# Kernel tuning notes

Hardware: AMD Instinct MI355X
Metric: run time of the kernel (lower is better)

Reference implementation:

```python
import jax, jax.numpy as jnp
import numpy as np

N = 16384
L = 4096  # n_locations

def setup_inputs() -> dict:
    key = jax.random.key(0)
    k1, k2, k3, k4 = jax.random.split(key, 4)
    w = jax.random.randint(k1, (N,), 0, L)
    z = jax.random.normal(k2, (N, L), dtype=jnp.float32)
    W = jax.random.normal(k3, (L, L), dtype=jnp.float32) * (1.0 / np.sqrt(L))
    b = jax.random.normal(k4, (L,), dtype=jnp.float32) * 0.01
    return {"w": w, "z": z, "W": W, "b": b}

def reference(w, z, W, b):
    # zw[i] = z[i, w[i]]
    zw = jnp.take_along_axis(z, w[:, None], axis=1)[:, 0]  # [N]
    # Original: inp = scatter(zw at column w); out = inp @ W.T + b
    # Mathematically: out[i, j] = zw[i] * W[j, w[i]] + b[j]
    out = zw[:, None] * W.T[w] + b  # [N, L]
    return out
```

## Files before the change

### kernel.cpp

```cpp
#include <hip/hip_runtime.h>

#define N_ROWS 16384
#define L_DIM  4096
#define CG     16
#define JT     1024
#define NBKT   (L_DIM / CG)
#define PITCH  (JT + 4)
#define CAP    1792

typedef float f32x4 __attribute__((ext_vector_type(4)));

__global__ __launch_bounds__(256, 2) void pnet_fused(
    const int* __restrict__ w,
    const float* __restrict__ z,
    const float* __restrict__ W,
    const float* __restrict__ b,
    float* __restrict__ out)
{
    __shared__ float tile[CG * PITCH];
    __shared__ int   list[CAP];
    __shared__ float zlist[CAP];
    __shared__ int   cnt;

    const int tid  = threadIdx.x;
    const int l0   = blockIdx.x * CG;
    const int j0   = blockIdx.y * JT;
    const int wid  = tid >> 6;
    const int lane = tid & 63;

    if (tid == 0) cnt = 0;

    f32x4 bb[4];
    #pragma unroll
    for (int k = 0; k < 4; ++k)
        bb[k] = *(const f32x4*)&b[j0 + (k * 64 + lane) * 4];

    __syncthreads();

    {
        const int q     = tid & 3;
        const int rbase = tid >> 2;
        #pragma unroll
        for (int it = 0; it < JT / 64; ++it) {
            const int r = rbase + it * 64;
            const f32x4 v = *(const f32x4*)&W[(size_t)(j0 + r) * L_DIM + l0 + 4 * q];
            tile[(4 * q + 0) * PITCH + r] = v.x;
            tile[(4 * q + 1) * PITCH + r] = v.y;
            tile[(4 * q + 2) * PITCH + r] = v.z;
            tile[(4 * q + 3) * PITCH + r] = v.w;
        }
    }

    #pragma unroll
    for (int s = 0; s < N_ROWS / 1024; ++s) {
        const int i0  = s * 1024 + tid * 4;
        const int4 wv = *(const int4*)&w[i0];
        const int vals[4] = {wv.x, wv.y, wv.z, wv.w};
        #pragma unroll
        for (int e = 0; e < 4; ++e) {
            const unsigned c = (unsigned)(vals[e] - l0);
            if (c < CG) {
                const int pos = atomicAdd(&cnt, 1);
                if (pos < CAP) list[pos] = (i0 + e) | ((int)c << 16);
            }
        }
    }

    __syncthreads();
    const int n     = cnt;
    const int nmain = n < CAP ? n : CAP;

    for (int e = tid; e < nmain; e += 256) {
        const int ent = list[e];
        const int i   = ent & 0xFFFF;
        const int c   = ent >> 16;
        zlist[e] = z[(size_t)i * L_DIM + l0 + c];
    }
    __syncthreads();

    for (int e = wid; e < nmain; e += 4) {
        const int   ent = list[e];
        const int   i   = ent & 0xFFFF;
        const int   c   = ent >> 16;
        const float zw  = zlist[e];
        const float* __restrict__ trow = &tile[c * PITCH];
        float*       __restrict__ orow = &out[(size_t)i * L_DIM + j0];
        #pragma unroll
        for (int k = 0; k < 4; ++k) {
            const int jj = (k * 64 + lane) * 4;
            const f32x4 wv4 = *(const f32x4*)&trow[jj];
            f32x4 o;
            o.x = fmaf(zw, wv4.x, bb[k].x);
            o.y = fmaf(zw, wv4.y, bb[k].y);
            o.z = fmaf(zw, wv4.z, bb[k].z);
            o.w = fmaf(zw, wv4.w, bb[k].w);
            __builtin_nontemporal_store(o, (f32x4*)&orow[jj]);
        }
    }

    if (n > CAP) {
        for (int p = 0; p < N_ROWS / 1024; ++p) {
            __syncthreads();
            if (tid == 0) cnt = 0;
            __syncthreads();
            const int i0  = p * 1024 + tid * 4;
            const int4 wv = *(const int4*)&w[i0];
            const int vals[4] = {wv.x, wv.y, wv.z, wv.w};
            #pragma unroll
            for (int e = 0; e < 4; ++e) {
                const unsigned c = (unsigned)(vals[e] - l0);
                if (c < CG) {
                    const int pos = atomicAdd(&cnt, 1);
                    list[pos]  = (i0 + e) | ((int)c << 16);
                    zlist[pos] = z[(size_t)(i0 + e) * L_DIM + vals[e]];
                }
            }
            __syncthreads();
            const int np = cnt;
            for (int e = wid; e < np; e += 4) {
                const int   ent = list[e];
                const int   i   = ent & 0xFFFF;
                const int   c   = ent >> 16;
                const float zw  = zlist[e];
                const float* __restrict__ trow = &tile[c * PITCH];
                float*       __restrict__ orow = &out[(size_t)i * L_DIM + j0];
                #pragma unroll
                for (int k = 0; k < 4; ++k) {
                    const int jj = (k * 64 + lane) * 4;
                    const f32x4 wv4 = *(const f32x4*)&trow[jj];
                    f32x4 o;
                    o.x = fmaf(zw, wv4.x, bb[k].x);
                    o.y = fmaf(zw, wv4.y, bb[k].y);
                    o.z = fmaf(zw, wv4.z, bb[k].z);
                    o.w = fmaf(zw, wv4.w, bb[k].w);
                    __builtin_nontemporal_store(o, (f32x4*)&orow[jj]);
                }
            }
        }
    }
}

extern "C" void kernel_launch(void* const* d_in, const int* in_sizes, int n_in,
                              void* d_out, int out_size, void* d_ws, size_t ws_size,
                              hipStream_t stream) {
    const int*   w = (const int*)d_in[0];
    const float* z = (const float*)d_in[1];
    const float* W = (const float*)d_in[2];
    const float* b = (const float*)d_in[3];
    float* out = (float*)d_out;

    dim3 grid(NBKT, L_DIM / JT);
    pnet_fused<<<grid, 256, 0, stream>>>(w, z, W, b, out);
}
```

Before: 75.91 us.

## Widen column tile to 2048, halve grid, shrink list capacity

Each block now covers 2048 output columns instead of 1024, so the grid shrinks to 512 blocks and each block scans the w array half as often per output column. The list capacity drops to 384, sized to the expected bucket count for uniform inputs, and address math moves to 32-bit. The overflow path now processes 256 rows per pass with plain stores. The larger LDS tile (~128KB) forces one block per CU, which lowers occupancy and latency hiding.

```diff
diff --git a/kernel.cpp b/kernel.cpp
--- a/kernel.cpp
+++ b/kernel.cpp
@@ -3,14 +3,13 @@
 #define N_ROWS 16384
 #define L_DIM  4096
 #define CG     16
-#define JT     1024
-#define NBKT   (L_DIM / CG)
+#define JT     2048
 #define PITCH  (JT + 4)
-#define CAP    1792
+#define CAP    384
 
 typedef float f32x4 __attribute__((ext_vector_type(4)));
 
-__global__ __launch_bounds__(256, 2) void pnet_fused(
+__global__ __launch_bounds__(256, 1) void pnet_fused(
     const int* __restrict__ w,
     const float* __restrict__ z,
     const float* __restrict__ W,
@@ -23,17 +22,18 @@
     __shared__ int   cnt;
 
     const int tid  = threadIdx.x;
-    const int l0   = blockIdx.x * CG;
-    const int j0   = blockIdx.y * JT;
+    const int g    = blockIdx.x >> 1;
+    const int l0   = g * CG;
+    const int j0   = (blockIdx.x & 1) * JT;
     const int wid  = tid >> 6;
     const int lane = tid & 63;
 
     if (tid == 0) cnt = 0;
 
-    f32x4 bb[4];
+    f32x4 bb[JT / 256];
     #pragma unroll
-    for (int k = 0; k < 4; ++k)
-        bb[k] = *(const f32x4*)&b[j0 + (k * 64 + lane) * 4];
+    for (int k = 0; k < JT / 256; ++k)
+        bb[k] = *(const f32x4*)&b[j0 + k * 256 + lane * 4];
 
     __syncthreads();
 
@@ -65,16 +65,13 @@
             }
         }
     }
-
     __syncthreads();
     const int n     = cnt;
     const int nmain = n < CAP ? n : CAP;
 
     for (int e = tid; e < nmain; e += 256) {
         const int ent = list[e];
-        const int i   = ent & 0xFFFF;
-        const int c   = ent >> 16;
-        zlist[e] = z[(size_t)i * L_DIM + l0 + c];
+        zlist[e] = z[(unsigned)((ent & 0xFFFF) * L_DIM) + (unsigned)(ent >> 16) + l0];
     }
     __syncthreads();
 
@@ -84,10 +81,10 @@
         const int   c   = ent >> 16;
         const float zw  = zlist[e];
         const float* __restrict__ trow = &tile[c * PITCH];
-        float*       __restrict__ orow = &out[(size_t)i * L_DIM + j0];
+        float*       __restrict__ orow = &out[(unsigned)(i * L_DIM) + j0];
         #pragma unroll
-        for (int k = 0; k < 4; ++k) {
-            const int jj = (k * 64 + lane) * 4;
+        for (int k = 0; k < JT / 256; ++k) {
+            const int jj = k * 256 + lane * 4;
             const f32x4 wv4 = *(const f32x4*)&trow[jj];
             f32x4 o;
             o.x = fmaf(zw, wv4.x, bb[k].x);
@@ -99,41 +96,37 @@
     }
 
     if (n > CAP) {
-        for (int p = 0; p < N_ROWS / 1024; ++p) {
+        for (int p = 0; p < N_ROWS / 256; ++p) {
             __syncthreads();
             if (tid == 0) cnt = 0;
             __syncthreads();
-            const int i0  = p * 1024 + tid * 4;
-            const int4 wv = *(const int4*)&w[i0];
-            const int vals[4] = {wv.x, wv.y, wv.z, wv.w};
-            #pragma unroll
-            for (int e = 0; e < 4; ++e) {
-                const unsigned c = (unsigned)(vals[e] - l0);
-                if (c < CG) {
-                    const int pos = atomicAdd(&cnt, 1);
-                    list[pos]  = (i0 + e) | ((int)c << 16);
-                    zlist[pos] = z[(size_t)(i0 + e) * L_DIM + vals[e]];
-                }
+            const int i  = p * 256 + tid;
+            const int wi = w[i];
+            const unsigned c = (unsigned)(wi - l0);
+            if (c < CG) {
+                const int pos = atomicAdd(&cnt, 1);
+                list[pos]  = i | ((int)c << 16);
+                zlist[pos] = z[(size_t)i * L_DIM + wi];
             }
             __syncthreads();
             const int np = cnt;
             for (int e = wid; e < np; e += 4) {
                 const int   ent = list[e];
-                const int   i   = ent & 0xFFFF;
-                const int   c   = ent >> 16;
+                const int   ii  = ent & 0xFFFF;
+                const int   c2  = ent >> 16;
                 const float zw  = zlist[e];
-                const float* __restrict__ trow = &tile[c * PITCH];
-                float*       __restrict__ orow = &out[(size_t)i * L_DIM + j0];
+                const float* __restrict__ trow = &tile[c2 * PITCH];
+                float*       __restrict__ orow = &out[(unsigned)(ii * L_DIM) + j0];
                 #pragma unroll
-                for (int k = 0; k < 4; ++k) {
-                    const int jj = (k * 64 + lane) * 4;
+                for (int k = 0; k < JT / 256; ++k) {
+                    const int jj = k * 256 + lane * 4;
                     const f32x4 wv4 = *(const f32x4*)&trow[jj];
                     f32x4 o;
                     o.x = fmaf(zw, wv4.x, bb[k].x);
                     o.y = fmaf(zw, wv4.y, bb[k].y);
                     o.z = fmaf(zw, wv4.z, bb[k].z);
                     o.w = fmaf(zw, wv4.w, bb[k].w);
-                    __builtin_nontemporal_store(o, (f32x4*)&orow[jj]);
+                    *(f32x4*)&orow[jj] = o;
                 }
             }
         }
@@ -149,6 +142,5 @@
     const float* b = (const float*)d_in[3];
     float* out = (float*)d_out;
 
-    dim3 grid(NBKT, L_DIM / JT);
-    pnet_fused<<<grid, 256, 0, stream>>>(w, z, W, b, out);
+    pnet_fused<<<512, 256, 0, stream>>>(w, z, W, b, out);
 }
```

Result: slower. 79.32 us (+4.5%).
